# Performance work log

Hardware: AMD Instinct MI355X
Metric: run time of the kernel (lower is better)

Reference implementation:

```python
import jax, jax.numpy as jnp
import numpy as np

D = 1024
H = 16
DK = D // H  # 64
CHUNK = 64
EPS = 1e-5


def setup_inputs() -> dict:
    key = jax.random.key(0)
    k1, k2, k3 = jax.random.split(key, 3)
    x = jax.random.normal(k1, (4, 4096, D), dtype=jnp.float32)
    W_qkv = jax.random.normal(k2, (D, 3 * D), dtype=jnp.float32) * 0.02
    W_o = jax.random.normal(k3, (D, D), dtype=jnp.float32) * 0.02
    return {"x": x, "W_qkv": W_qkv, "W_o": W_o}


def _layernorm_noaffine(k):
    mu = jnp.mean(k, axis=-1, keepdims=True)
    var = jnp.mean((k - mu) ** 2, axis=-1, keepdims=True)  # biased var, torch LayerNorm
    return (k - mu) / jnp.sqrt(var + EPS)


def _linear_attn(x, W_qkv, W_o):
    B, L, Dm = x.shape
    qkv = (x @ W_qkv).reshape(B, L, 3, H, DK)
    q, k, v = qkv[:, :, 0], qkv[:, :, 1], qkv[:, :, 2]
    k = _layernorm_noaffine(k)

    nC = L // CHUNK
    # [nC, B, C, H, DK] for scan over chunks
    to_chunks = lambda t: t.reshape(B, nC, CHUNK, H, DK).transpose(1, 0, 2, 3, 4)
    qc, kc, vc = to_chunks(q), to_chunks(k), to_chunks(v)

    causal = jnp.tril(jnp.ones((CHUNK, CHUNK), dtype=bool))  # s <= t inclusive

    def step(S, chunk):
        q_c, k_c, v_c = chunk  # each [B, C, H, DK]
        # inter-chunk: y_t += S_prev @ q_t
        inter = jnp.einsum('bhde,bthe->bthd', S, q_c)
        # intra-chunk: y_t += sum_{s<=t} (k_s . q_t) v_s
        scores = jnp.einsum('bthd,bshd->bhts', q_c, k_c)
        scores = jnp.where(causal, scores, 0.0)
        intra = jnp.einsum('bhts,bshd->bthd', scores, v_c)
        # state update: S += sum_t v_t k_t^T
        S = S + jnp.einsum('bthd,bthe->bhde', v_c, k_c)
        return S, inter + intra

    S0 = jnp.zeros((B, H, DK, DK), dtype=x.dtype)
    _, ys = jax.lax.scan(step, S0, (qc, kc, vc))  # ys: [nC, B, C, H, DK]
    y = ys.transpose(1, 0, 2, 3, 4).reshape(B, L, Dm)
    return y @ W_o


def reference(x, W_qkv, W_o):
    return _linear_attn(x, W_qkv, W_o)
```

## Files before the change

kernel.cpp:

```cpp
#include <hip/hip_runtime.h>

#define EPS 1e-5f

typedef __attribute__((ext_vector_type(8))) short s16x8;
typedef __attribute__((ext_vector_type(4))) float f4;

__device__ __forceinline__ short f2bf(float f) {
  union { float f; unsigned u; } x; x.f = f;
  unsigned r = x.u + 0x7fffu + ((x.u >> 16) & 1u);
  return (short)(r >> 16);
}
__device__ __forceinline__ float bf2f(short s) {
  union { unsigned u; float f; } x; x.u = ((unsigned)(unsigned short)s) << 16;
  return x.f;
}
__device__ __forceinline__ void gll16(const short* g, short* l) {
  __builtin_amdgcn_global_load_lds((const __attribute__((address_space(1))) void*)g,
                                   (__attribute__((address_space(3))) void*)l, 16, 0, 0);
}

__global__ __launch_bounds__(256) void prep(
    const float* __restrict__ x, const float* __restrict__ Wqkv,
    const float* __restrict__ Wo,
    short* __restrict__ xb, short* __restrict__ WqkvT, short* __restrict__ WoT)
{
  __shared__ float tile[32][33];
  const int bid = blockIdx.x;
  if (bid < 8192) {
    const size_t i = ((size_t)bid * 256 + threadIdx.x) * 8;
    const float4* p = reinterpret_cast<const float4*>(x + i);
    float4 a = p[0], b = p[1];
    union { uint4 v; short s[8]; } o;
    o.s[0] = f2bf(a.x); o.s[1] = f2bf(a.y); o.s[2] = f2bf(a.z); o.s[3] = f2bf(a.w);
    o.s[4] = f2bf(b.x); o.s[5] = f2bf(b.y); o.s[6] = f2bf(b.z); o.s[7] = f2bf(b.w);
    *reinterpret_cast<uint4*>(xb + i) = o.v;
    return;
  }
  const float* W; short* WT; int K, N, t;
  if (bid < 11264) { W = Wqkv; WT = WqkvT; K = 1024; N = 3072; t = bid - 8192;  }
  else             { W = Wo;   WT = WoT;   K = 1024; N = 1024; t = bid - 11264; }
  const int nblk = N >> 5;
  const int n0 = (t % nblk) * 32, k0 = (t / nblk) * 32;
  const int tx = threadIdx.x & 31, ty = threadIdx.x >> 5;
  #pragma unroll
  for (int i = 0; i < 4; i++) {
    int r = ty + i * 8;
    tile[r][tx] = W[(size_t)(k0 + r) * N + n0 + tx];
  }
  __syncthreads();
  #pragma unroll
  for (int i = 0; i < 4; i++) {
    int r = ty + i * 8;
    WT[(size_t)(n0 + r) * K + k0 + tx] = f2bf(tile[tx][r]);
  }
}

__global__ __launch_bounds__(256) void gemm_qkv_v4(
    const short* __restrict__ A, const short* __restrict__ BT,
    short* __restrict__ qb, short* __restrict__ kb, short* __restrict__ vb)
{
  __shared__ __align__(16) short lds[8192];
  short* As = lds;
  short* Bs = lds + 4096;

  const int p = blockIdx.x;
  const int slot = p >> 3;
  const int strip = (p & 7) + 8 * (slot / 24);
  const int nb = slot % 24;
  const int m0 = strip * 128, n0 = nb * 128;

  const int tid = threadIdx.x;
  const int w = tid >> 6, lane = tid & 63, quad = lane >> 4, l16 = lane & 15;
  const int wm = (w >> 1) << 6, wn = (w & 1) << 6;

  f4 acc[4][4];
  #pragma unroll
  for (int i = 0; i < 4; i++)
    #pragma unroll
    for (int j = 0; j < 4; j++) acc[i][j] = {0.f, 0.f, 0.f, 0.f};

  const int row = w * 32 + (lane >> 2), ofs = (lane & 3) << 3;

  for (int k0 = 0; k0 < 1024; k0 += 32) {
    __syncthreads();
    gll16(A + (size_t)(m0 + row) * 1024 + k0 + ofs, &As[(w * 32) * 32]);
    gll16(A + (size_t)(m0 + row + 16) * 1024 + k0 + ofs, &As[(w * 32 + 16) * 32]);
    gll16(BT + (size_t)(n0 + row) * 1024 + k0 + ofs, &Bs[(w * 32) * 32]);
    gll16(BT + (size_t)(n0 + row + 16) * 1024 + k0 + ofs, &Bs[(w * 32 + 16) * 32]);
    __syncthreads();
    s16x8 afr[4], bfr[4];
    #pragma unroll
    for (int t = 0; t < 4; t++)
      afr[t] = *reinterpret_cast<const s16x8*>(&As[(wm + t * 16 + l16) * 32 + quad * 8]);
    #pragma unroll
    for (int t = 0; t < 4; t++)
      bfr[t] = *reinterpret_cast<const s16x8*>(&Bs[(wn + t * 16 + l16) * 32 + quad * 8]);
    #pragma unroll
    for (int ti = 0; ti < 4; ti++)
      #pragma unroll
      for (int tj = 0; tj < 4; tj++)
        acc[ti][tj] = __builtin_amdgcn_mfma_f32_16x16x32_bf16(afr[ti], bfr[tj], acc[ti][tj], 0, 0, 0);
  }

  __syncthreads();
  short* st = &lds[w * 16 * 72];
  const int j0 = n0 + wn;
  const int sq = j0 >> 10;
  const int hh = (j0 >> 6) & 15;
  short* dbuf = (sq == 0) ? qb : (sq == 1) ? kb : vb;
  const int r2 = lane >> 3, c8 = (lane & 7) << 3;
  #pragma unroll
  for (int ti = 0; ti < 4; ti++) {
    #pragma unroll
    for (int tj = 0; tj < 4; tj++)
      #pragma unroll
      for (int r = 0; r < 4; r++)
        st[(quad * 4 + r) * 72 + tj * 16 + l16] = f2bf(acc[ti][tj][r]);
    #pragma unroll
    for (int h2 = 0; h2 < 2; h2++) {
      int rr = h2 * 8 + r2;
      int i = m0 + wm + ti * 16 + rr;
      int bb = i >> 12, ll = i & 4095;
      uint4 val = *reinterpret_cast<const uint4*>(&st[rr * 72 + c8]);
      *reinterpret_cast<uint4*>(&dbuf[(((size_t)(bb * 16 + hh)) * 4096 + ll) * 64 + c8]) = val;
    }
  }
}

__global__ __launch_bounds__(256) void ln_k(short* __restrict__ kbuf)
{
  const int row = blockIdx.x * 4 + (threadIdx.x >> 6);
  const int lane = threadIdx.x & 63;
  const size_t idx = (size_t)row * 64 + lane;
  float v = bf2f(kbuf[idx]);
  float s = v, s2 = v * v;
  #pragma unroll
  for (int off = 32; off; off >>= 1) {
    s += __shfl_xor(s, off);
    s2 += __shfl_xor(s2, off);
  }
  float mean = s * (1.f / 64.f);
  float var = s2 * (1.f / 64.f) - mean * mean;
  float rstd = rsqrtf(var + EPS);
  kbuf[idx] = f2bf((v - mean) * rstd);
}

__global__ __launch_bounds__(256) void chunk_outer(
    const short* __restrict__ kb, const short* __restrict__ vb,
    short* __restrict__ G)
{
  __shared__ __align__(16) short kT[64 * 72];
  __shared__ __align__(16) short vT[64 * 72];
  const int bh = blockIdx.x >> 6, c = blockIdx.x & 63;
  const int tid = threadIdx.x;
  const int w = tid >> 6, lane = tid & 63, quad = lane >> 4, l16 = lane & 15;
  const int srow = tid >> 2, sseg = (tid & 3) << 4;
  const size_t base = (size_t)bh * 262144 + (size_t)(c * 64 + srow) * 64 + sseg;

  {
    const float4* kp = reinterpret_cast<const float4*>(kb + base);
    union { float4 v[2]; short s[16]; } ku;
    ku.v[0] = kp[0]; ku.v[1] = kp[1];
    float kv[16]; float s = 0.f, s2 = 0.f;
    #pragma unroll
    for (int i = 0; i < 16; i++) { kv[i] = bf2f(ku.s[i]); s += kv[i]; s2 += kv[i] * kv[i]; }
    s += __shfl_xor(s, 1);  s2 += __shfl_xor(s2, 1);
    s += __shfl_xor(s, 2);  s2 += __shfl_xor(s2, 2);
    float mean = s * (1.f / 64.f);
    float var = s2 * (1.f / 64.f) - mean * mean;
    float rstd = rsqrtf(var + EPS);
    #pragma unroll
    for (int i = 0; i < 16; i++) kT[(sseg + i) * 72 + srow] = f2bf((kv[i] - mean) * rstd);
    const float4* vp = reinterpret_cast<const float4*>(vb + base);
    union { float4 v[2]; short s[16]; } vu;
    vu.v[0] = vp[0]; vu.v[1] = vp[1];
    #pragma unroll
    for (int i = 0; i < 16; i++) vT[(sseg + i) * 72 + srow] = vu.s[i];
  }
  __syncthreads();
  s16x8 va0 = *reinterpret_cast<const s16x8*>(&vT[(w * 16 + l16) * 72 + quad * 8]);
  s16x8 va1 = *reinterpret_cast<const s16x8*>(&vT[(w * 16 + l16) * 72 + 32 + quad * 8]);
  short* Gc = G + ((size_t)blockIdx.x) * 4096;
  #pragma unroll
  for (int tj = 0; tj < 4; tj++) {
    s16x8 kb0 = *reinterpret_cast<const s16x8*>(&kT[(tj * 16 + l16) * 72 + quad * 8]);
    s16x8 kb1 = *reinterpret_cast<const s16x8*>(&kT[(tj * 16 + l16) * 72 + 32 + quad * 8]);
    f4 z = {0.f, 0.f, 0.f, 0.f};
    z = __builtin_amdgcn_mfma_f32_16x16x32_bf16(va0, kb0, z, 0, 0, 0);
    z = __builtin_amdgcn_mfma_f32_16x16x32_bf16(va1, kb1, z, 0, 0, 0);
    #pragma unroll
    for (int r = 0; r < 4; r++)
      Gc[(w * 16 + quad * 4 + r) * 64 + tj * 16 + l16] = f2bf(z[r]);
  }
}

__global__ __launch_bounds__(128) void prefix_S(short* __restrict__ G)
{
  const int bh = blockIdx.x >> 3, rg = blockIdx.x & 7;
  const size_t base = (size_t)bh * 262144 + rg * 512 + threadIdx.x * 4;
  float s0 = 0.f, s1 = 0.f, s2 = 0.f, s3 = 0.f;
  for (int c = 0; c < 64; c++) {
    short* p = G + base + (size_t)c * 4096;
    union { uint2 v; short s[4]; } gu;
    gu.v = *reinterpret_cast<const uint2*>(p);
    float g0 = bf2f(gu.s[0]), g1 = bf2f(gu.s[1]), g2 = bf2f(gu.s[2]), g3 = bf2f(gu.s[3]);
    union { uint2 v; short s[4]; } su;
    su.s[0] = f2bf(s0); su.s[1] = f2bf(s1); su.s[2] = f2bf(s2); su.s[3] = f2bf(s3);
    *reinterpret_cast<uint2*>(p) = su.v;
    s0 += g0; s1 += g1; s2 += g2; s3 += g3;
  }
}

__global__ __launch_bounds__(256) void chunk_out(
    const short* __restrict__ qb, const short* __restrict__ kb,
    const short* __restrict__ vb, const short* __restrict__ S,
    short* __restrict__ yb)
{
  __shared__ __align__(16) short vT[64 * 72];
  __shared__ __align__(16) short Ps[64 * 72];
  const int bh = blockIdx.x >> 6, c = blockIdx.x & 63;
  const int b = bh >> 4, h = bh & 15;
  const int tid = threadIdx.x;
  const int w = tid >> 6, lane = tid & 63, quad = lane >> 4, l16 = lane & 15;
  const int srow = tid >> 2, sseg = (tid & 3) << 4;
  const size_t base = (size_t)bh * 262144 + (size_t)c * 4096;

  {
    const float4* vp = reinterpret_cast<const float4*>(vb + base + (size_t)srow * 64 + sseg);
    union { float4 v[2]; short s[16]; } vu;
    vu.v[0] = vp[0]; vu.v[1] = vp[1];
    #pragma unroll
    for (int i = 0; i < 16; i++) vT[(sseg + i) * 72 + srow] = vu.s[i];
  }
  s16x8 qa[4][2], kf[2], sf[2];
  #pragma unroll
  for (int ti = 0; ti < 4; ti++)
    #pragma unroll
    for (int kh = 0; kh < 2; kh++)
      qa[ti][kh] = *reinterpret_cast<const s16x8*>(
          qb + base + (size_t)(ti * 16 + l16) * 64 + kh * 32 + quad * 8);
  #pragma unroll
  for (int kh = 0; kh < 2; kh++) {
    kf[kh] = *reinterpret_cast<const s16x8*>(
        kb + base + (size_t)(w * 16 + l16) * 64 + kh * 32 + quad * 8);
    sf[kh] = *reinterpret_cast<const s16x8*>(
        S + base + (size_t)(w * 16 + l16) * 64 + kh * 32 + quad * 8);
  }
  {
    float kv[16]; float s = 0.f, s2 = 0.f;
    #pragma unroll
    for (int kh = 0; kh < 2; kh++)
      #pragma unroll
      for (int i = 0; i < 8; i++) {
        float f = bf2f(kf[kh][i]); kv[kh * 8 + i] = f; s += f; s2 += f * f;
      }
    s += __shfl_xor(s, 16);  s2 += __shfl_xor(s2, 16);
    s += __shfl_xor(s, 32);  s2 += __shfl_xor(s2, 32);
    float mean = s * (1.f / 64.f);
    float var = s2 * (1.f / 64.f) - mean * mean;
    float rstd = rsqrtf(var + EPS);
    #pragma unroll
    for (int kh = 0; kh < 2; kh++)
      #pragma unroll
      for (int i = 0; i < 8; i++)
        kf[kh][i] = f2bf((kv[kh * 8 + i] - mean) * rstd);
  }
  __syncthreads();
  #pragma unroll
  for (int ti = 0; ti < 4; ti++) {
    f4 z = {0.f, 0.f, 0.f, 0.f};
    z = __builtin_amdgcn_mfma_f32_16x16x32_bf16(qa[ti][0], kf[0], z, 0, 0, 0);
    z = __builtin_amdgcn_mfma_f32_16x16x32_bf16(qa[ti][1], kf[1], z, 0, 0, 0);
    #pragma unroll
    for (int r = 0; r < 4; r++) {
      int t = ti * 16 + quad * 4 + r;
      int s = w * 16 + l16;
      Ps[t * 72 + s] = (s <= t) ? f2bf(z[r]) : (short)0;
    }
  }
  __syncthreads();
  s16x8 vf0 = *reinterpret_cast<const s16x8*>(&vT[(w * 16 + l16) * 72 + quad * 8]);
  s16x8 vf1 = *reinterpret_cast<const s16x8*>(&vT[(w * 16 + l16) * 72 + 32 + quad * 8]);
  #pragma unroll
  for (int ti = 0; ti < 4; ti++) {
    f4 z = {0.f, 0.f, 0.f, 0.f};
    s16x8 p0 = *reinterpret_cast<const s16x8*>(&Ps[(ti * 16 + l16) * 72 + quad * 8]);
    s16x8 p1 = *reinterpret_cast<const s16x8*>(&Ps[(ti * 16 + l16) * 72 + 32 + quad * 8]);
    z = __builtin_amdgcn_mfma_f32_16x16x32_bf16(p0, vf0, z, 0, 0, 0);
    z = __builtin_amdgcn_mfma_f32_16x16x32_bf16(p1, vf1, z, 0, 0, 0);
    z = __builtin_amdgcn_mfma_f32_16x16x32_bf16(qa[ti][0], sf[0], z, 0, 0, 0);
    z = __builtin_amdgcn_mfma_f32_16x16x32_bf16(qa[ti][1], sf[1], z, 0, 0, 0);
    #pragma unroll
    for (int r = 0; r < 4; r++) {
      int t = ti * 16 + quad * 4 + r;
      int d = w * 16 + l16;
      yb[(((size_t)b * 4096) + c * 64 + t) * 1024 + h * 64 + d] = f2bf(z[r]);
    }
  }
}

__global__ __launch_bounds__(256) void gemm_out_v3(
    const short* __restrict__ A, const short* __restrict__ BT, float* __restrict__ C)
{
  __shared__ __align__(16) short As[128 * 32];
  __shared__ __align__(16) short Bs[128 * 32];
  const int p = blockIdx.x;
  const int slot = p >> 3;
  const int strip = (p & 7) + 8 * (slot >> 3);
  const int nb = slot & 7;
  const int m0 = strip * 128, n0 = nb * 128;
  const int tid = threadIdx.x;
  const int w = tid >> 6, lane = tid & 63, quad = lane >> 4, l16 = lane & 15;
  const int wm = (w >> 1) << 6, wn = (w & 1) << 6;

  f4 acc[4][4];
  #pragma unroll
  for (int i = 0; i < 4; i++)
    #pragma unroll
    for (int j = 0; j < 4; j++) acc[i][j] = {0.f, 0.f, 0.f, 0.f};

  const int row = w * 32 + (lane >> 2), ofs = (lane & 3) << 3;

  for (int k0 = 0; k0 < 1024; k0 += 32) {
    __syncthreads();
    gll16(A + (size_t)(m0 + row) * 1024 + k0 + ofs, &As[(w * 32) * 32]);
    gll16(A + (size_t)(m0 + row + 16) * 1024 + k0 + ofs, &As[(w * 32 + 16) * 32]);
    gll16(BT + (size_t)(n0 + row) * 1024 + k0 + ofs, &Bs[(w * 32) * 32]);
    gll16(BT + (size_t)(n0 + row + 16) * 1024 + k0 + ofs, &Bs[(w * 32 + 16) * 32]);
    __syncthreads();
    s16x8 afr[4], bfr[4];
    #pragma unroll
    for (int t = 0; t < 4; t++)
      afr[t] = *reinterpret_cast<const s16x8*>(&As[(wm + t * 16 + l16) * 32 + quad * 8]);
    #pragma unroll
    for (int t = 0; t < 4; t++)
      bfr[t] = *reinterpret_cast<const s16x8*>(&Bs[(wn + t * 16 + l16) * 32 + quad * 8]);
    #pragma unroll
    for (int ti = 0; ti < 4; ti++)
      #pragma unroll
      for (int tj = 0; tj < 4; tj++)
        acc[ti][tj] = __builtin_amdgcn_mfma_f32_16x16x32_bf16(afr[ti], bfr[tj], acc[ti][tj], 0, 0, 0);
  }
  #pragma unroll
  for (int ti = 0; ti < 4; ti++)
    #pragma unroll
    for (int tj = 0; tj < 4; tj++)
      #pragma unroll
      for (int r = 0; r < 4; r++) {
        int i = m0 + wm + ti * 16 + quad * 4 + r;
        int j = n0 + wn + tj * 16 + l16;
        C[(size_t)i * 1024 + j] = acc[ti][tj][r];
      }
}

__global__ __launch_bounds__(256) void gemm_qkv_r1(
    const float* __restrict__ A, const float* __restrict__ B,
    short* __restrict__ qb, short* __restrict__ kb, short* __restrict__ vb)
{
  __shared__ __align__(16) short As[128 * 40];
  __shared__ __align__(16) short Bs[128 * 40];
  const int n0 = blockIdx.x * 128;
  const int m0 = blockIdx.y * 128;
  const int tid = threadIdx.x;
  const int w = tid >> 6, lane = tid & 63, quad = lane >> 4, l16 = lane & 15;
  const int wm = (w >> 1) << 6, wn = (w & 1) << 6;
  f4 acc[4][4];
  #pragma unroll
  for (int i = 0; i < 4; i++)
    #pragma unroll
    for (int j = 0; j < 4; j++) acc[i][j] = {0.f, 0.f, 0.f, 0.f};
  const int arow = tid >> 1, aseg = (tid & 1) << 4;
  const int brow = tid >> 3, bseg = (tid & 7) << 4;
  for (int k0 = 0; k0 < 1024; k0 += 32) {
    __syncthreads();
    {
      const float4* ap = reinterpret_cast<const float4*>(A + (size_t)(m0 + arow) * 1024 + k0 + aseg);
      union { float4 v[4]; float f[16]; } af;
      af.v[0] = ap[0]; af.v[1] = ap[1]; af.v[2] = ap[2]; af.v[3] = ap[3];
      union { float4 v[2]; short s[16]; } ao;
      #pragma unroll
      for (int i = 0; i < 16; i++) ao.s[i] = f2bf(af.f[i]);
      float4* dst = reinterpret_cast<float4*>(&As[arow * 40 + aseg]);
      dst[0] = ao.v[0]; dst[1] = ao.v[1];
    }
    {
      const float4* bp = reinterpret_cast<const float4*>(B + (size_t)(k0 + brow) * 3072 + n0 + bseg);
      union { float4 v[4]; float f[16]; } bu;
      bu.v[0] = bp[0]; bu.v[1] = bp[1]; bu.v[2] = bp[2]; bu.v[3] = bp[3];
      #pragma unroll
      for (int i = 0; i < 16; i++) Bs[(bseg + i) * 40 + brow] = f2bf(bu.f[i]);
    }
    __syncthreads();
    s16x8 afr[4], bfr[4];
    #pragma unroll
    for (int t = 0; t < 4; t++)
      afr[t] = *reinterpret_cast<const s16x8*>(&As[(wm + t * 16 + l16) * 40 + quad * 8]);
    #pragma unroll
    for (int t = 0; t < 4; t++)
      bfr[t] = *reinterpret_cast<const s16x8*>(&Bs[(wn + t * 16 + l16) * 40 + quad * 8]);
    #pragma unroll
    for (int ti = 0; ti < 4; ti++)
      #pragma unroll
      for (int tj = 0; tj < 4; tj++)
        acc[ti][tj] = __builtin_amdgcn_mfma_f32_16x16x32_bf16(afr[ti], bfr[tj], acc[ti][tj], 0, 0, 0);
  }
  const int sq = n0 >> 10;
  short* dbuf = (sq == 0) ? qb : (sq == 1) ? kb : vb;
  #pragma unroll
  for (int ti = 0; ti < 4; ti++)
    #pragma unroll
    for (int tj = 0; tj < 4; tj++)
      #pragma unroll
      for (int r = 0; r < 4; r++) {
        int i = m0 + wm + ti * 16 + quad * 4 + r;
        int j = n0 + wn + tj * 16 + l16;
        int hh = (j >> 6) & 15, dd = j & 63;
        int bb = i >> 12, ll = i & 4095;
        dbuf[(((size_t)(bb * 16 + hh)) * 4096 + ll) * 64 + dd] = f2bf(acc[ti][tj][r]);
      }
}

__global__ __launch_bounds__(256) void scan_chunks_r1(
    const short* __restrict__ qb, const short* __restrict__ kb,
    const short* __restrict__ vb, short* __restrict__ yb)
{
  __shared__ __align__(16) short qs[64 * 72];
  __shared__ __align__(16) short ks[64 * 72];
  __shared__ __align__(16) short kT[64 * 72];
  __shared__ __align__(16) short vT[64 * 72];
  __shared__ __align__(16) short Sb[64 * 72];
  __shared__ __align__(16) short Ps[64 * 72];
  const int bh = blockIdx.x;
  const int b = bh >> 4, h = bh & 15;
  const int tid = threadIdx.x;
  const int w = tid >> 6, lane = tid & 63, quad = lane >> 4, l16 = lane & 15;
  const int srow = tid >> 2, sseg = (tid & 3) << 4;
  const size_t base = (size_t)bh * 4096 * 64;
  f4 accS[4];
  #pragma unroll
  for (int i = 0; i < 4; i++) accS[i] = {0.f, 0.f, 0.f, 0.f};
  for (int c = 0; c < 64; c++) {
    __syncthreads();
    {
      size_t g = base + ((size_t)(c * 64 + srow)) * 64 + sseg;
      const float4* qp = reinterpret_cast<const float4*>(qb + g);
      float4 q0 = qp[0], q1 = qp[1];
      *reinterpret_cast<float4*>(&qs[srow * 72 + sseg]) = q0;
      *reinterpret_cast<float4*>(&qs[srow * 72 + sseg + 8]) = q1;
      const float4* kp = reinterpret_cast<const float4*>(kb + g);
      union { float4 v[2]; short s[16]; } ku;
      ku.v[0] = kp[0]; ku.v[1] = kp[1];
      *reinterpret_cast<float4*>(&ks[srow * 72 + sseg]) = ku.v[0];
      *reinterpret_cast<float4*>(&ks[srow * 72 + sseg + 8]) = ku.v[1];
      #pragma unroll
      for (int i = 0; i < 16; i++) kT[(sseg + i) * 72 + srow] = ku.s[i];
      const float4* vp = reinterpret_cast<const float4*>(vb + g);
      union { float4 v[2]; short s[16]; } vu;
      vu.v[0] = vp[0]; vu.v[1] = vp[1];
      #pragma unroll
      for (int i = 0; i < 16; i++) vT[(sseg + i) * 72 + srow] = vu.s[i];
    }
    #pragma unroll
    for (int ti = 0; ti < 4; ti++)
      #pragma unroll
      for (int r = 0; r < 4; r++)
        Sb[(ti * 16 + quad * 4 + r) * 72 + w * 16 + l16] = f2bf(accS[ti][r]);
    __syncthreads();
    s16x8 qa[4][2];
    #pragma unroll
    for (int ti = 0; ti < 4; ti++)
      #pragma unroll
      for (int kh = 0; kh < 2; kh++)
        qa[ti][kh] = *reinterpret_cast<const s16x8*>(&qs[(ti * 16 + l16) * 72 + kh * 32 + quad * 8]);
    s16x8 kf[2];
    #pragma unroll
    for (int kh = 0; kh < 2; kh++)
      kf[kh] = *reinterpret_cast<const s16x8*>(&ks[(w * 16 + l16) * 72 + kh * 32 + quad * 8]);
    #pragma unroll
    for (int ti = 0; ti < 4; ti++) {
      f4 z = {0.f, 0.f, 0.f, 0.f};
      z = __builtin_amdgcn_mfma_f32_16x16x32_bf16(qa[ti][0], kf[0], z, 0, 0, 0);
      z = __builtin_amdgcn_mfma_f32_16x16x32_bf16(qa[ti][1], kf[1], z, 0, 0, 0);
      #pragma unroll
      for (int r = 0; r < 4; r++) {
        int t = ti * 16 + quad * 4 + r;
        int s = w * 16 + l16;
        Ps[t * 72 + s] = (s <= t) ? f2bf(z[r]) : (short)0;
      }
    }
    __syncthreads();
    s16x8 vf[2], sf[2];
    #pragma unroll
    for (int kh = 0; kh < 2; kh++) {
      vf[kh] = *reinterpret_cast<const s16x8*>(&vT[(w * 16 + l16) * 72 + kh * 32 + quad * 8]);
      sf[kh] = *reinterpret_cast<const s16x8*>(&Sb[(w * 16 + l16) * 72 + kh * 32 + quad * 8]);
    }
    #pragma unroll
    for (int ti = 0; ti < 4; ti++) {
      f4 z = {0.f, 0.f, 0.f, 0.f};
      s16x8 p0 = *reinterpret_cast<const s16x8*>(&Ps[(ti * 16 + l16) * 72 + quad * 8]);
      s16x8 p1 = *reinterpret_cast<const s16x8*>(&Ps[(ti * 16 + l16) * 72 + 32 + quad * 8]);
      z = __builtin_amdgcn_mfma_f32_16x16x32_bf16(p0, vf[0], z, 0, 0, 0);
      z = __builtin_amdgcn_mfma_f32_16x16x32_bf16(p1, vf[1], z, 0, 0, 0);
      z = __builtin_amdgcn_mfma_f32_16x16x32_bf16(qa[ti][0], sf[0], z, 0, 0, 0);
      z = __builtin_amdgcn_mfma_f32_16x16x32_bf16(qa[ti][1], sf[1], z, 0, 0, 0);
      #pragma unroll
      for (int r = 0; r < 4; r++) {
        int t = ti * 16 + quad * 4 + r;
        int d = w * 16 + l16;
        yb[(((size_t)b * 4096) + c * 64 + t) * 1024 + h * 64 + d] = f2bf(z[r]);
      }
    }
    s16x8 ku0 = *reinterpret_cast<const s16x8*>(&kT[(w * 16 + l16) * 72 + quad * 8]);
    s16x8 ku1 = *reinterpret_cast<const s16x8*>(&kT[(w * 16 + l16) * 72 + 32 + quad * 8]);
    #pragma unroll
    for (int ti = 0; ti < 4; ti++) {
      s16x8 va0 = *reinterpret_cast<const s16x8*>(&vT[(ti * 16 + l16) * 72 + quad * 8]);
      s16x8 va1 = *reinterpret_cast<const s16x8*>(&vT[(ti * 16 + l16) * 72 + 32 + quad * 8]);
      accS[ti] = __builtin_amdgcn_mfma_f32_16x16x32_bf16(va0, ku0, accS[ti], 0, 0, 0);
      accS[ti] = __builtin_amdgcn_mfma_f32_16x16x32_bf16(va1, ku1, accS[ti], 0, 0, 0);
    }
  }
}

__global__ __launch_bounds__(256) void gemm_out_r1(
    const short* __restrict__ A, const float* __restrict__ B, float* __restrict__ C)
{
  __shared__ __align__(16) short As[128 * 40];
  __shared__ __align__(16) short Bs[128 * 40];
  const int n0 = blockIdx.x * 128;
  const int m0 = blockIdx.y * 128;
  const int tid = threadIdx.x;
  const int w = tid >> 6, lane = tid & 63, quad = lane >> 4, l16 = lane & 15;
  const int wm = (w >> 1) << 6, wn = (w & 1) << 6;
  f4 acc[4][4];
  #pragma unroll
  for (int i = 0; i < 4; i++)
    #pragma unroll
    for (int j = 0; j < 4; j++) acc[i][j] = {0.f, 0.f, 0.f, 0.f};
  const int arow = tid >> 1, aseg = (tid & 1) << 4;
  const int brow = tid >> 3, bseg = (tid & 7) << 4;
  for (int k0 = 0; k0 < 1024; k0 += 32) {
    __syncthreads();
    {
      const float4* ap = reinterpret_cast<const float4*>(A + (size_t)(m0 + arow) * 1024 + k0 + aseg);
      float4 a0 = ap[0], a1 = ap[1];
      float4* dst = reinterpret_cast<float4*>(&As[arow * 40 + aseg]);
      dst[0] = a0; dst[1] = a1;
    }
    {
      const float4* bp = reinterpret_cast<const float4*>(B + (size_t)(k0 + brow) * 1024 + n0 + bseg);
      union { float4 v[4]; float f[16]; } bu;
      bu.v[0] = bp[0]; bu.v[1] = bp[1]; bu.v[2] = bp[2]; bu.v[3] = bp[3];
      #pragma unroll
      for (int i = 0; i < 16; i++) Bs[(bseg + i) * 40 + brow] = f2bf(bu.f[i]);
    }
    __syncthreads();
    s16x8 afr[4], bfr[4];
    #pragma unroll
    for (int t = 0; t < 4; t++)
      afr[t] = *reinterpret_cast<const s16x8*>(&As[(wm + t * 16 + l16) * 40 + quad * 8]);
    #pragma unroll
    for (int t = 0; t < 4; t++)
      bfr[t] = *reinterpret_cast<const s16x8*>(&Bs[(wn + t * 16 + l16) * 40 + quad * 8]);
    #pragma unroll
    for (int ti = 0; ti < 4; ti++)
      #pragma unroll
      for (int tj = 0; tj < 4; tj++)
        acc[ti][tj] = __builtin_amdgcn_mfma_f32_16x16x32_bf16(afr[ti], bfr[tj], acc[ti][tj], 0, 0, 0);
  }
  #pragma unroll
  for (int ti = 0; ti < 4; ti++)
    #pragma unroll
    for (int tj = 0; tj < 4; tj++)
      #pragma unroll
      for (int r = 0; r < 4; r++) {
        int i = m0 + wm + ti * 16 + quad * 4 + r;
        int j = n0 + wn + tj * 16 + l16;
        C[(size_t)i * 1024 + j] = acc[ti][tj][r];
      }
}

extern "C" void kernel_launch(void* const* d_in, const int* in_sizes, int n_in,
                              void* d_out, int out_size, void* d_ws, size_t ws_size,
                              hipStream_t stream) {
  const float* x    = (const float*)d_in[0];
  const float* Wqkv = (const float*)d_in[1];
  const float* Wo   = (const float*)d_in[2];
  float* out = (float*)d_out;

  short* qb = (short*)d_ws;
  short* kb = qb + (size_t)16777216;
  short* vb = kb + (size_t)16777216;
  short* yb = vb + (size_t)16777216;

  const size_t NEED = 176160768;
  if (ws_size >= NEED) {
    short* Gs    = yb + (size_t)16777216;
    short* WqkvT = Gs + (size_t)16777216;
    short* WoT   = WqkvT + (size_t)3145728;
    short* xb    = Gs;

    prep          <<<dim3(12288),   256, 0, stream>>>(x, Wqkv, Wo, xb, WqkvT, WoT);
    gemm_qkv_v4   <<<dim3(3072),    256, 0, stream>>>(xb, WqkvT, qb, kb, vb);
    chunk_outer   <<<dim3(4096),    256, 0, stream>>>(kb, vb, Gs);
    prefix_S      <<<dim3(512),     128, 0, stream>>>(Gs);
    chunk_out     <<<dim3(4096),    256, 0, stream>>>(qb, kb, vb, Gs, yb);
    gemm_out_v3   <<<dim3(1024),    256, 0, stream>>>(yb, WoT, out);
  } else {
    gemm_qkv_r1   <<<dim3(24, 128), 256, 0, stream>>>(x, Wqkv, qb, kb, vb);
    ln_k          <<<dim3(65536),   256, 0, stream>>>(kb);
    scan_chunks_r1<<<dim3(64),      256, 0, stream>>>(qb, kb, vb, yb);
    gemm_out_r1   <<<dim3(8, 128),  256, 0, stream>>>(yb, Wo, out);
  }
}
```

Baseline: 354.5 us.

## Replace projection GEMMs with 256x256-tile 8-wave double-buffered LDS pipeline

Adds new QKV and output projection GEMM kernels that use 256x256 tiles, 512 threads and 128KB of dynamic LDS split into two buffers. The next K-tile is staged with global_load_lds while MFMAs run on the current one, using explicit barriers, waitcnts and setprio. The larger tiles and the overlap are meant to raise data reuse and hide global load latency. They depend on raising the dynamic shared memory limit; if that call fails, the code falls back to the old kernels.

```diff
diff --git a/kernel.cpp b/kernel.cpp
--- a/kernel.cpp
+++ b/kernel.cpp
@@ -18,6 +18,10 @@
   __builtin_amdgcn_global_load_lds((const __attribute__((address_space(1))) void*)g,
                                    (__attribute__((address_space(3))) void*)l, 16, 0, 0);
 }
+
+#define BAR() asm volatile("s_barrier" ::: "memory")
+#define LGKM0() do { asm volatile("s_waitcnt lgkmcnt(0)" ::: "memory"); \
+                     __builtin_amdgcn_sched_barrier(0); } while (0)
 
 __global__ __launch_bounds__(256) void prep(
     const float* __restrict__ x, const float* __restrict__ Wqkv,
@@ -53,6 +57,177 @@
     int r = ty + i * 8;
     WT[(size_t)(n0 + r) * K + k0 + tx] = f2bf(tile[tx][r]);
   }
+}
+
+__device__ __forceinline__ void stage_slice(const short* __restrict__ G, short* dstbase,
+                                            int row0, int kcol, int rowgrp, int panel, int lane) {
+  short* dst = dstbase + panel * 8192 + rowgrp * 512;
+  const short* src = G + (size_t)(row0 + rowgrp * 16 + (lane >> 2)) * 1024
+                       + kcol + panel * 32 + (((lane & 3) << 3) ^ ((lane >> 5) << 4));
+  gll16(src, dst);
+}
+
+template<bool STAGE>
+__device__ __forceinline__ void ktile8p(
+    const short* ldsAc, const short* ldsBc, short* ldsAn, short* ldsBn,
+    const short* __restrict__ A, const short* __restrict__ BT,
+    int m0, int n0, int knext,
+    int w, int lane, int wm, int wn, int quad, int l16,
+    f4 (&acc)[8][4])
+{
+  s16x8 bfr[4][2];
+  const int co = (quad << 3) ^ ((l16 >> 3) << 4);
+  #pragma unroll
+  for (int p = 0; p < 4; ++p) {
+    s16x8 a00, a01, a10, a11;
+    {
+      const int r0 = (wm * 128 + p * 32 + l16) * 32;
+      a00 = *reinterpret_cast<const s16x8*>(&ldsAc[r0 + co]);
+      a01 = *reinterpret_cast<const s16x8*>(&ldsAc[8192 + r0 + co]);
+      a10 = *reinterpret_cast<const s16x8*>(&ldsAc[r0 + 512 + co]);
+      a11 = *reinterpret_cast<const s16x8*>(&ldsAc[8192 + r0 + 512 + co]);
+    }
+    if (p == 0) {
+      #pragma unroll
+      for (int nf = 0; nf < 4; ++nf) {
+        const int rb = (wn * 64 + nf * 16 + l16) * 32;
+        bfr[nf][0] = *reinterpret_cast<const s16x8*>(&ldsBc[rb + co]);
+        bfr[nf][1] = *reinterpret_cast<const s16x8*>(&ldsBc[8192 + rb + co]);
+      }
+    }
+    if (STAGE) {
+      if (p == 0)      { stage_slice(BT, ldsBn, n0, knext, w,     0, lane); stage_slice(BT, ldsBn, n0, knext, w,     1, lane); }
+      else if (p == 1) { stage_slice(BT, ldsBn, n0, knext, 8 + w, 0, lane); stage_slice(BT, ldsBn, n0, knext, 8 + w, 1, lane); }
+      else if (p == 2) { const int rg = (w & 3) + ((w >> 2) << 3);
+                         stage_slice(A, ldsAn, m0, knext, rg, 0, lane); stage_slice(A, ldsAn, m0, knext, rg, 1, lane); }
+      else             { const int rg = 4 + (w & 3) + ((w >> 2) << 3);
+                         stage_slice(A, ldsAn, m0, knext, rg, 0, lane); stage_slice(A, ldsAn, m0, knext, rg, 1, lane); }
+    }
+    BAR();
+    LGKM0();
+    __builtin_amdgcn_s_setprio(1);
+    #pragma unroll
+    for (int nf = 0; nf < 4; ++nf) {
+      acc[2*p  ][nf] = __builtin_amdgcn_mfma_f32_16x16x32_bf16(a00, bfr[nf][0], acc[2*p  ][nf], 0, 0, 0);
+      acc[2*p  ][nf] = __builtin_amdgcn_mfma_f32_16x16x32_bf16(a01, bfr[nf][1], acc[2*p  ][nf], 0, 0, 0);
+      acc[2*p+1][nf] = __builtin_amdgcn_mfma_f32_16x16x32_bf16(a10, bfr[nf][0], acc[2*p+1][nf], 0, 0, 0);
+      acc[2*p+1][nf] = __builtin_amdgcn_mfma_f32_16x16x32_bf16(a11, bfr[nf][1], acc[2*p+1][nf], 0, 0, 0);
+    }
+    __builtin_amdgcn_s_setprio(0);
+    if (p == 1) {
+      if (STAGE) asm volatile("s_waitcnt vmcnt(4)" ::: "memory");
+      else       asm volatile("s_waitcnt vmcnt(0)" ::: "memory");
+    }
+    if (p == 3 && STAGE) asm volatile("s_waitcnt vmcnt(2)" ::: "memory");
+    BAR();
+  }
+}
+
+#define GEMM8P_PROLOGUE()                                                            \
+  stage_slice(BT, Bb0, n0, 0, w,     0, lane); stage_slice(BT, Bb0, n0, 0, w,     1, lane); \
+  stage_slice(BT, Bb0, n0, 0, 8 + w, 0, lane); stage_slice(BT, Bb0, n0, 0, 8 + w, 1, lane); \
+  { const int rg = (w & 3) + ((w >> 2) << 3);                                        \
+    stage_slice(A, Ab0, m0, 0, rg, 0, lane); stage_slice(A, Ab0, m0, 0, rg, 1, lane); } \
+  { const int rg = 4 + (w & 3) + ((w >> 2) << 3);                                    \
+    stage_slice(A, Ab0, m0, 0, rg, 0, lane); stage_slice(A, Ab0, m0, 0, rg, 1, lane); } \
+  asm volatile("s_waitcnt vmcnt(2)" ::: "memory");                                   \
+  BAR()
+
+#define GEMM8P_MAINLOOP()                                                            \
+  _Pragma("unroll 1")                                                                \
+  for (int t = 0; t < 14; t += 2) {                                                  \
+    ktile8p<true>(Ab0, Bb0, Ab1, Bb1, A, BT, m0, n0, (t + 1) << 6, w, lane, wm, wn, quad, l16, acc); \
+    ktile8p<true>(Ab1, Bb1, Ab0, Bb0, A, BT, m0, n0, (t + 2) << 6, w, lane, wm, wn, quad, l16, acc); \
+  }                                                                                  \
+  ktile8p<true >(Ab0, Bb0, Ab1, Bb1, A, BT, m0, n0, 15 << 6, w, lane, wm, wn, quad, l16, acc); \
+  ktile8p<false>(Ab1, Bb1, Ab0, Bb0, A, BT, m0, n0, 0,       w, lane, wm, wn, quad, l16, acc)
+
+__global__ __launch_bounds__(512, 2) void gemm_qkv_8p(
+    const short* __restrict__ A, const short* __restrict__ BT,
+    short* __restrict__ qb, short* __restrict__ kb, short* __restrict__ vb)
+{
+  extern __shared__ __align__(16) short lds[];
+  short* Ab0 = lds;           short* Ab1 = lds + 16384;
+  short* Bb0 = lds + 32768;   short* Bb1 = lds + 49152;
+
+  const int pid = blockIdx.x;
+  const int wg = (pid & 7) * 96 + (pid >> 3);
+  const int mb = wg / 12, nb = wg % 12;
+  const int m0 = mb * 256, n0 = nb * 256;
+
+  const int tid = threadIdx.x;
+  const int w = tid >> 6, lane = tid & 63, quad = lane >> 4, l16 = lane & 15;
+  const int wm = w >> 2, wn = w & 3;
+
+  f4 acc[8][4];
+  #pragma unroll
+  for (int i = 0; i < 8; i++)
+    #pragma unroll
+    for (int j = 0; j < 4; j++) acc[i][j] = {0.f, 0.f, 0.f, 0.f};
+
+  GEMM8P_PROLOGUE();
+  GEMM8P_MAINLOOP();
+
+  __syncthreads();
+  short* st = lds + w * 1152;
+  const int j0 = n0 + wn * 64;
+  const int sq = j0 >> 10;
+  const int hh = (j0 >> 6) & 15;
+  short* dbuf = (sq == 0) ? qb : (sq == 1) ? kb : vb;
+  const int r2 = lane >> 3, c8 = (lane & 7) << 3;
+  #pragma unroll
+  for (int mf = 0; mf < 8; ++mf) {
+    #pragma unroll
+    for (int nf = 0; nf < 4; ++nf)
+      #pragma unroll
+      for (int r = 0; r < 4; ++r)
+        st[(quad * 4 + r) * 72 + nf * 16 + l16] = f2bf(acc[mf][nf][r]);
+    #pragma unroll
+    for (int h2 = 0; h2 < 2; ++h2) {
+      int rr = h2 * 8 + r2;
+      int i = m0 + wm * 128 + mf * 16 + rr;
+      int bb = i >> 12, ll = i & 4095;
+      uint4 val = *reinterpret_cast<const uint4*>(&st[rr * 72 + c8]);
+      *reinterpret_cast<uint4*>(&dbuf[(((size_t)(bb * 16 + hh)) * 4096 + ll) * 64 + c8]) = val;
+    }
+  }
+}
+
+__global__ __launch_bounds__(512, 2) void gemm_out_8p(
+    const short* __restrict__ A, const short* __restrict__ BT, float* __restrict__ C)
+{
+  extern __shared__ __align__(16) short lds[];
+  short* Ab0 = lds;           short* Ab1 = lds + 16384;
+  short* Bb0 = lds + 32768;   short* Bb1 = lds + 49152;
+
+  const int pid = blockIdx.x;
+  const int wg = (pid & 7) * 32 + (pid >> 3);
+  const int mb = wg >> 2, nb = wg & 3;
+  const int m0 = mb * 256, n0 = nb * 256;
+
+  const int tid = threadIdx.x;
+  const int w = tid >> 6, lane = tid & 63, quad = lane >> 4, l16 = lane & 15;
+  const int wm = w >> 2, wn = w & 3;
+
+  f4 acc[8][4];
+  #pragma unroll
+  for (int i = 0; i < 8; i++)
+    #pragma unroll
+    for (int j = 0; j < 4; j++) acc[i][j] = {0.f, 0.f, 0.f, 0.f};
+
+  GEMM8P_PROLOGUE();
+  GEMM8P_MAINLOOP();
+
+  #pragma unroll
+  for (int mf = 0; mf < 8; ++mf)
+    #pragma unroll
+    for (int nf = 0; nf < 4; ++nf)
+      #pragma unroll
+      for (int r = 0; r < 4; ++r) {
+        int i = m0 + wm * 128 + mf * 16 + quad * 4 + r;
+        int j = n0 + wn * 64 + nf * 16 + l16;
+        C[(size_t)i * 1024 + j] = acc[mf][nf][r];
+      }
 }
 
 __global__ __launch_bounds__(256) void gemm_qkv_v4(
@@ -601,12 +776,27 @@
     short* WoT   = WqkvT + (size_t)3145728;
     short* xb    = Gs;
 
+    static int use8p = -1;
+    if (use8p < 0) {
+      hipError_t e1 = hipFuncSetAttribute((const void*)gemm_qkv_8p,
+          hipFuncAttributeMaxDynamicSharedMemorySize, 131072);
+      hipError_t e2 = hipFuncSetAttribute((const void*)gemm_out_8p,
+          hipFuncAttributeMaxDynamicSharedMemorySize, 131072);
+      use8p = (e1 == hipSuccess && e2 == hipSuccess) ? 1 : 0;
+    }
+
     prep          <<<dim3(12288),   256, 0, stream>>>(x, Wqkv, Wo, xb, WqkvT, WoT);
-    gemm_qkv_v4   <<<dim3(3072),    256, 0, stream>>>(xb, WqkvT, qb, kb, vb);
+    if (use8p)
+      gemm_qkv_8p <<<dim3(768),     512, 131072, stream>>>(xb, WqkvT, qb, kb, vb);
+    else
+      gemm_qkv_v4 <<<dim3(3072),    256, 0, stream>>>(xb, WqkvT, qb, kb, vb);
     chunk_outer   <<<dim3(4096),    256, 0, stream>>>(kb, vb, Gs);
     prefix_S      <<<dim3(512),     128, 0, stream>>>(Gs);
     chunk_out     <<<dim3(4096),    256, 0, stream>>>(qb, kb, vb, Gs, yb);
-    gemm_out_v3   <<<dim3(1024),    256, 0, stream>>>(yb, WoT, out);
+    if (use8p)
+      gemm_out_8p <<<dim3(256),     512, 131072, stream>>>(yb, WoT, out);
+    else
+      gemm_out_v3 <<<dim3(1024),    256, 0, stream>>>(yb, WoT, out);
   } else {
     gemm_qkv_r1   <<<dim3(24, 128), 256, 0, stream>>>(x, Wqkv, qb, kb, vb);
     ln_k          <<<dim3(65536),   256, 0, stream>>>(kb);
```

Measured after the change: 315.1 us. -11.1%, faster.
